# Kernel tuning notes

Measured on AMD Instinct MI355X. Metric: run time of the kernel, lower is better.

The kernel has to match this reference:

```python
import jax, jax.numpy as jnp
import numpy as np

EPS = 1e-6
H = 8  # num_heads

def _ln(x, gamma, beta):
    mu = jnp.mean(x, axis=-1, keepdims=True)
    var = jnp.mean(jnp.square(x - mu), axis=-1, keepdims=True)
    return (x - mu) * jax.lax.rsqrt(var + EPS) * gamma + beta

def setup_inputs() -> dict:
    key = jax.random.key(0)
    ks = jax.random.split(key, 10)
    b, n_sink, n_src = 2, 1024, 4096
    sink_dim, src_dim, hid = 512, 512, 512
    s = 0.02
    return {
        "sink": jax.random.normal(ks[0], (b, n_sink, sink_dim), jnp.float32),
        "source": jax.random.normal(ks[1], (b, n_src, src_dim), jnp.float32),
        "gamma_s": jnp.ones((sink_dim,), jnp.float32),
        "beta_s": jnp.zeros((sink_dim,), jnp.float32),
        "gamma_c": jnp.ones((src_dim,), jnp.float32),
        "beta_c": jnp.zeros((src_dim,), jnp.float32),
        "Wq": jax.random.normal(ks[2], (sink_dim, hid), jnp.float32) * s,
        "bq": jnp.zeros((hid,), jnp.float32),
        "Wkv": jax.random.normal(ks[3], (src_dim, 2 * hid), jnp.float32) * s,
        "bkv": jnp.zeros((2 * hid,), jnp.float32),
        "Wo": jax.random.normal(ks[4], (hid, sink_dim), jnp.float32) * s,
        "bo": jnp.zeros((sink_dim,), jnp.float32),
    }

def reference(sink, source, gamma_s, beta_s, gamma_c, beta_c, Wq, bq, Wkv, bkv, Wo, bo):
    b, n_sink, _ = sink.shape
    n_src = source.shape[1]
    hid = Wq.shape[1]
    d = hid // H
    scale = d ** -0.5
    # pre-norm
    s = _ln(sink, gamma_s, beta_s)
    c = _ln(source, gamma_c, beta_c)
    # projections -> [b, h, n, d]
    q = (s @ Wq + bq).reshape(b, n_sink, H, d).transpose(0, 2, 1, 3)
    kv = c @ Wkv + bkv
    k, v = jnp.split(kv, 2, axis=-1)
    k = k.reshape(b, n_src, H, d).transpose(0, 2, 1, 3)
    v = v.reshape(b, n_src, H, d).transpose(0, 2, 1, 3)
    sim = jnp.einsum('bhid,bhjd->bhij', q, k) * scale  # [b,h,i,j]
    # sink competition: softmax over query axis i, then renormalize over keys j
    attn = jax.nn.softmax(sim, axis=-2) + EPS
    attn = attn / jnp.sum(attn, axis=-1, keepdims=True)
    out = jnp.einsum('bhij,bhjd->bhid', attn, v)
    out = out.transpose(0, 2, 1, 3).reshape(b, n_sink, hid)
    return out @ Wo + bo
```

## Files before the change

### kernel.cpp

```cpp
#include <hip/hip_runtime.h>
#include <hip/hip_bf16.h>
#include <math.h>

#define EPS 1e-6f
#define NSINK 1024
#define NSRC 4096
#define DIM 512
#define NH 8
#define HD 64
#define BATCH 2
#define VROWS 65
#define QSCALE 0.18033688011112042f

#if __has_builtin(__builtin_amdgcn_permlane32_swap) && __has_builtin(__builtin_amdgcn_permlane16_swap)
#define HAVE_PERMLANE 1
#else
#define HAVE_PERMLANE 0
#endif

typedef unsigned short u16;
typedef __attribute__((ext_vector_type(8))) short short8;
typedef __attribute__((ext_vector_type(4))) float f32x4;

__device__ inline float fast_exp2(float x) {
#if __has_builtin(__builtin_amdgcn_exp2f)
    return __builtin_amdgcn_exp2f(x);
#else
    return exp2f(x);
#endif
}
__device__ inline float fast_rcp(float x) {
#if __has_builtin(__builtin_amdgcn_rcpf)
    return __builtin_amdgcn_rcpf(x);
#else
    return 1.0f / x;
#endif
}
__device__ inline u16 f2bf(float x) {
    union { float f; unsigned u; } v; v.f = x;
    unsigned r = v.u + 0x7fffu + ((v.u >> 16) & 1u);
    return (u16)(r >> 16);
}
__device__ inline float bf2f(u16 h) {
    union { unsigned u; float f; } v; v.u = ((unsigned)h) << 16;
    return v.f;
}
__device__ inline unsigned pk_bf16(float a, float b) {
    union { __hip_bfloat162 h; unsigned u; } v;
    v.h = __float22bfloat162_rn(make_float2(a, b));
    return v.u;
}
__device__ inline f32x4 mfma16(short8 a, short8 b, f32x4 c) {
    return __builtin_amdgcn_mfma_f32_16x16x32_bf16(a, b, c, 0, 0, 0);
}
__device__ inline short8 ldfrag(const u16* base, int stride, int lane) {
    return *(const short8*)(base + (size_t)(lane & 15) * stride + ((lane >> 4) << 3));
}

__device__ inline void gld16(const u16* g, u16* l) {
    __builtin_amdgcn_global_load_lds(
        (const __attribute__((address_space(1))) unsigned*)g,
        (__attribute__((address_space(3))) unsigned*)l, 16, 0, 0);
}

template<int TM>
__device__ inline void stage_tile(u16* lds, const u16* gsrc, int K, int t) {
    #pragma unroll
    for (int it = 0; it < TM / 32; ++it) {
        int m = it * 32 + (t >> 3);
        int c = (t & 7) ^ (m & 7);
        gld16(gsrc + (size_t)m * K + c * 8,
              lds + it * 2048 + (t >> 6) * 512);
    }
}
__device__ inline short8 rdfrag(const u16* tile, int fbase, int cbase, int lane) {
    int m = fbase + (lane & 15);
    int c = (cbase + (lane >> 4)) ^ (m & 7);
    return *(const short8*)(tile + (size_t)m * 64 + c * 8);
}

#if HAVE_PERMLANE
__device__ inline short8 pa_frag(const f32x4 sA, const f32x4 sB) {
    unsigned A0 = pk_bf16(sA[0], sA[1]);
    unsigned A1 = pk_bf16(sA[2], sA[3]);
    unsigned B0 = pk_bf16(sB[0], sB[1]);
    unsigned B1 = pk_bf16(sB[2], sB[3]);
    auto c0 = __builtin_amdgcn_permlane32_swap(A0, B0, false, false);
    auto c1 = __builtin_amdgcn_permlane32_swap(A1, B1, false, false);
    auto d0 = __builtin_amdgcn_permlane16_swap(c0[0], c0[1], false, false);
    auto d1 = __builtin_amdgcn_permlane16_swap(c1[0], c1[1], false, false);
    union { unsigned u[4]; short8 s8; } r;
    r.u[0] = d0[0]; r.u[1] = d1[0]; r.u[2] = d0[1]; r.u[3] = d1[1];
    return r.s8;
}
#endif

__global__ __launch_bounds__(256) void prep(
    const float* __restrict__ sink, const float* __restrict__ source,
    const float* __restrict__ gs, const float* __restrict__ bs,
    const float* __restrict__ gc, const float* __restrict__ bc,
    const float* __restrict__ Wq, const float* __restrict__ Wkv,
    const float* __restrict__ Wo,
    u16* __restrict__ sh, u16* __restrict__ ch,
    u16* __restrict__ wqT, u16* __restrict__ wkvT, u16* __restrict__ woT)
{
    int row = blockIdx.x;
    int t = threadIdx.x;
    if (row >= BATCH * (NSINK + NSRC)) {
        int n = row - BATCH * (NSINK + NSRC);
        const float* W; u16* T; int N; int nn;
        if (n < 512)       { W = Wq;  T = wqT;  N = 512;  nn = n; }
        else if (n < 1536) { W = Wkv; T = wkvT; N = 1024; nn = n - 512; }
        else               { W = Wo;  T = woT;  N = 512;  nn = n - 1536; }
        for (int k = t; k < 512; k += 256)
            T[(size_t)nn * 512 + k] = f2bf(W[(size_t)k * N + nn]);
        return;
    }
    const float* xr; const float* g; const float* be; u16* y;
    if (row < BATCH * NSINK) {
        xr = sink + (size_t)row * DIM; g = gs; be = bs; y = sh + (size_t)row * DIM;
    } else {
        int rr = row - BATCH * NSINK;
        xr = source + (size_t)rr * DIM; g = gc; be = bc; y = ch + (size_t)rr * DIM;
    }
    float v0 = xr[t], v1 = xr[t + 256];
    float s = v0 + v1, sq = v0 * v0 + v1 * v1;
    #pragma unroll
    for (int off = 32; off > 0; off >>= 1) {
        s  += __shfl_down(s, off, 64);
        sq += __shfl_down(sq, off, 64);
    }
    __shared__ float rsm[4], rq[4];
    int wave = t >> 6;
    if ((t & 63) == 0) { rsm[wave] = s; rq[wave] = sq; }
    __syncthreads();
    s  = rsm[0] + rsm[1] + rsm[2] + rsm[3];
    sq = rq[0] + rq[1] + rq[2] + rq[3];
    float mu = s * (1.0f / DIM);
    float var = sq * (1.0f / DIM) - mu * mu;
    float a = var + EPS;
    float r = rsqrtf(a);
    r = r * (1.5f - 0.5f * a * r * r);
    y[t]       = f2bf((v0 - mu) * r * g[t] + be[t]);
    y[t + 256] = f2bf((v1 - mu) * r * g[t + 256] + be[t + 256]);
}

template<int MODE, int TM, int TN, int SWZ>
__global__ __launch_bounds__(256) void gemm1(
    const u16* __restrict__ A, const u16* __restrict__ BT,
    const float* __restrict__ bias, int K,
    float* __restrict__ cf, u16* __restrict__ o1, u16* __restrict__ o2)
{
    constexpr int FM = TM / 32, FN = TN / 32;
    __shared__ u16 As[2][TM * 64];
    __shared__ u16 Bs[2][TN * 64];
    int t = threadIdx.x;
    int wave = t >> 6, lane = t & 63;
    int wr = wave >> 1, wc = wave & 1;
    int m0, n0;
    if constexpr (SWZ) {
        int id = blockIdx.x;
        int slot = id >> 3;
        m0 = ((id & 7) * 8 + (slot & 7)) * TM;
        n0 = (slot >> 3) * TN;
    } else {
        m0 = blockIdx.y * TM;
        n0 = blockIdx.x * TN;
    }

    f32x4 acc[FM][FN] = {};
    stage_tile<TM>(As[0], A + (size_t)m0 * K, K, t);
    stage_tile<TN>(Bs[0], BT + (size_t)n0 * K, K, t);
    __syncthreads();
    int nt = K >> 6;
    int cur = 0;
    for (int kt = 0; kt < nt; ++kt) {
        if (kt + 1 < nt) {
            stage_tile<TM>(As[cur ^ 1], A + (size_t)m0 * K + (kt + 1) * 64, K, t);
            stage_tile<TN>(Bs[cur ^ 1], BT + (size_t)n0 * K + (kt + 1) * 64, K, t);
        }
        #pragma unroll
        for (int kk = 0; kk < 2; ++kk) {
            short8 af[FM], bf[FN];
            #pragma unroll
            for (int f = 0; f < FM; ++f)
                af[f] = rdfrag(As[cur], wr * (TM / 2) + f * 16, kk * 4, lane);
            #pragma unroll
            for (int f = 0; f < FN; ++f)
                bf[f] = rdfrag(Bs[cur], wc * (TN / 2) + f * 16, kk * 4, lane);
            #pragma unroll
            for (int i = 0; i < FM; ++i)
                #pragma unroll
                for (int j = 0; j < FN; ++j)
                    acc[i][j] = mfma16(af[i], bf[j], acc[i][j]);
        }
        __syncthreads();
        cur ^= 1;
    }

    #pragma unroll
    for (int i = 0; i < FM; ++i)
        #pragma unroll
        for (int j = 0; j < FN; ++j)
            #pragma unroll
            for (int r = 0; r < 4; ++r) {
                int m = m0 + wr * (TM / 2) + i * 16 + (lane >> 4) * 4 + r;
                int n = n0 + wc * (TN / 2) + j * 16 + (lane & 15);
                float v = acc[i][j][r] + bias[n];
                if (MODE == 0) {
                    cf[(size_t)m * DIM + n] = v;
                } else if (MODE == 1) {
                    int b = m >> 10, ii = m & 1023;
                    int h = n >> 6, d = n & 63;
                    o1[((size_t)(b * NH + h) * NSINK + ii) * HD + d] = f2bf(v * QSCALE);
                } else {
                    int b = m >> 12, jj = m & 4095;
                    if (n < DIM) {
                        int h = n >> 6, d = n & 63;
                        o1[((size_t)(b * NH + h) * NSRC + jj) * HD + d] = f2bf(v);
                    } else {
                        int nn = n - DIM;
                        int h = nn >> 6, d = nn & 63;
                        o2[((size_t)(b * NH + h) * HD + d) * NSRC + jj] = f2bf(v);
                    }
                }
            }
}

__global__ __launch_bounds__(256, 4) void pass_a(const u16* __restrict__ q,
    const u16* __restrict__ k, float* __restrict__ part)
{
    int id = blockIdx.x;
    int slot = id >> 3;
    int bh = (id & 7) + 8 * (slot >> 6);
    int rem = slot & 63;
    int ic = rem >> 4;
    int t = threadIdx.x, wave = t >> 6, lane = t & 63;
    int j0 = (rem & 15) * 256 + wave * 64;
    const u16* qb = q + (size_t)bh * NSINK * HD;
    const u16* kb = k + (size_t)bh * NSRC * HD;

    __shared__ u16 Qs[2][64 * 64];

    short8 kf[4][2];
    #pragma unroll
    for (int jf = 0; jf < 4; ++jf)
        #pragma unroll
        for (int kc = 0; kc < 2; ++kc)
            kf[jf][kc] = ldfrag(kb + (size_t)(j0 + jf * 16) * HD + kc * 32, HD, lane);

    float csum[4] = {};
    stage_tile<64>(Qs[0], qb + (size_t)(ic * 256) * HD, HD, t);
    __syncthreads();
    int cur = 0;
    for (int ii = 0; ii < 4; ++ii) {
        if (ii + 1 < 4)
            stage_tile<64>(Qs[cur ^ 1], qb + (size_t)(ic * 256 + (ii + 1) * 64) * HD, HD, t);
        #pragma unroll
        for (int f = 0; f < 4; ++f) {
            short8 q0 = rdfrag(Qs[cur], f * 16, 0, lane);
            short8 q1 = rdfrag(Qs[cur], f * 16, 4, lane);
            f32x4 s[4] = {};
            #pragma unroll
            for (int jf = 0; jf < 4; ++jf) s[jf] = mfma16(q0, kf[jf][0], s[jf]);
            #pragma unroll
            for (int jf = 0; jf < 4; ++jf) s[jf] = mfma16(q1, kf[jf][1], s[jf]);
            #pragma unroll
            for (int jf = 0; jf < 4; ++jf)
                csum[jf] += fast_exp2(s[jf][0]) + fast_exp2(s[jf][1])
                          + fast_exp2(s[jf][2]) + fast_exp2(s[jf][3]);
        }
        __syncthreads();
        cur ^= 1;
    }
    #pragma unroll
    for (int jf = 0; jf < 4; ++jf) {
        csum[jf] += __shfl_xor(csum[jf], 16, 64);
        csum[jf] += __shfl_xor(csum[jf], 32, 64);
    }
    if (lane < 16)
        #pragma unroll
        for (int jf = 0; jf < 4; ++jf)
            part[((size_t)ic * BATCH * NH + bh) * NSRC + j0 + jf * 16 + lane] = csum[jf];
}

__global__ __launch_bounds__(256) void csred(const float* __restrict__ part,
    float* __restrict__ rcs)
{
    int x = blockIdx.x * 256 + threadIdx.x;
    const int S = BATCH * NH * NSRC;
    float cs = part[x] + part[x + S] + part[x + 2 * S] + part[x + 3 * S];
    rcs[x] = fast_rcp(cs);
}

__global__ __launch_bounds__(256) void vscale2(const u16* __restrict__ vTh,
    const float* __restrict__ rcs, float* __restrict__ vs, u16* __restrict__ vT2)
{
    int d = blockIdx.x;
    int bh = blockIdx.y;
    const float* rc = rcs + (size_t)bh * NSRC;
    u16* dst = vT2 + ((size_t)bh * VROWS + d) * NSRC;
    if (d == 64) {
        for (int j = threadIdx.x; j < NSRC; j += 256) dst[j] = f2bf(rc[j]);
        return;
    }
    const u16* src = vTh + ((size_t)bh * HD + d) * NSRC;
    float acc = 0.f;
    for (int j = threadIdx.x; j < NSRC; j += 256) {
        float v = bf2f(src[j]);
        acc += v;
        dst[j] = f2bf(v * rc[j]);
    }
    #pragma unroll
    for (int off = 32; off > 0; off >>= 1) acc += __shfl_down(acc, off, 64);
    __shared__ float r4[4];
    if ((threadIdx.x & 63) == 0) r4[threadIdx.x >> 6] = acc;
    __syncthreads();
    if (threadIdx.x == 0) vs[bh * HD + d] = r4[0] + r4[1] + r4[2] + r4[3];
}

__global__ __launch_bounds__(256, 3) void pass_b(const u16* __restrict__ q,
    const u16* __restrict__ k, const u16* __restrict__ vT2,
    u16* __restrict__ pvb, float* __restrict__ rs)
{
    int id = blockIdx.x;
    int slot = id >> 3;
    int bh = (id & 7) + 8 * (slot >> 5);
    int rem = slot & 31;
    int split = rem >> 3;
    int i0 = (rem & 7) * 128;
    int t = threadIdx.x, wave = t >> 6, lane = t & 63;
    const u16* qb = q + (size_t)bh * NSINK * HD;
    const u16* kb = k + (size_t)bh * NSRC * HD;
    const u16* vb = vT2 + (size_t)bh * VROWS * NSRC;

    __shared__ u16 Ks[2][64 * 64];
    __shared__ u16 Vs[2][64 * 64];
    __shared__ alignas(16) u16 Rcs[2][64];
#if !HAVE_PERMLANE
    __shared__ alignas(16) u16 pbuf[4][2][16 * 76];
#endif

    short8 qf[2][2];
    #pragma unroll
    for (int fi = 0; fi < 2; ++fi)
        #pragma unroll
        for (int kc = 0; kc < 2; ++kc)
            qf[fi][kc] = ldfrag(qb + (size_t)(i0 + wave * 32 + fi * 16) * HD + kc * 32, HD, lane);

    auto stage = [&](int buf, int jt) {
        int j0 = split * (NSRC / 4) + jt * 64;
        stage_tile<64>(Ks[buf], kb + (size_t)j0 * HD, HD, t);
        stage_tile<64>(Vs[buf], vb + j0, NSRC, t);
        if (t < 8) gld16(vb + (size_t)64 * NSRC + j0 + t * 8, Rcs[buf]);
    };

    f32x4 o[2][5] = {};
    stage(0, 0);
    __syncthreads();
    int cur = 0;
    for (int jt = 0; jt < 16; ++jt) {
        if (jt + 1 < 16) stage(cur ^ 1, jt + 1);
        f32x4 s[2][4] = {};
        #pragma unroll
        for (int kc = 0; kc < 2; ++kc)
            #pragma unroll
            for (int jf = 0; jf < 4; ++jf) {
                short8 kf = rdfrag(Ks[cur], jf * 16, kc * 4, lane);
                s[0][jf] = mfma16(kf, qf[0][kc], s[0][jf]);
                s[1][jf] = mfma16(kf, qf[1][kc], s[1][jf]);
            }
        #pragma unroll
        for (int fi = 0; fi < 2; ++fi)
            #pragma unroll
            for (int jf = 0; jf < 4; ++jf)
                #pragma unroll
                for (int r = 0; r < 4; ++r)
                    s[fi][jf][r] = fast_exp2(s[fi][jf][r]);
#if !HAVE_PERMLANE
        #pragma unroll
        for (int fi = 0; fi < 2; ++fi)
            #pragma unroll
            for (int jf = 0; jf < 4; ++jf) {
                uint2 w;
                w.x = pk_bf16(s[fi][jf][0], s[fi][jf][1]);
                w.y = pk_bf16(s[fi][jf][2], s[fi][jf][3]);
                *(uint2*)&pbuf[wave][fi][(size_t)(lane & 15) * 76 + jf * 16 + (lane >> 4) * 4] = w;
            }
#endif
        short8 z = {};
        #pragma unroll
        for (int jc = 0; jc < 2; ++jc) {
#if HAVE_PERMLANE
            short8 pa0 = pa_frag(s[0][2 * jc], s[0][2 * jc + 1]);
            short8 pa1 = pa_frag(s[1][2 * jc], s[1][2 * jc + 1]);
#else
            short8 pa0 = *(const short8*)&pbuf[wave][0][(size_t)(lane & 15) * 76 + jc * 32 + (lane >> 4) * 8];
            short8 pa1 = *(const short8*)&pbuf[wave][1][(size_t)(lane & 15) * 76 + jc * 32 + (lane >> 4) * 8];
#endif
            #pragma unroll
            for (int df = 0; df < 4; ++df) {
                short8 vf = rdfrag(Vs[cur], df * 16, jc * 4, lane);
                o[0][df] = mfma16(pa0, vf, o[0][df]);
                o[1][df] = mfma16(pa1, vf, o[1][df]);
            }
            short8 b5 = z;
            if ((lane & 15) == 0)
                b5 = *(const short8*)&Rcs[cur][jc * 32 + (lane >> 4) * 8];
            o[0][4] = mfma16(pa0, b5, o[0][4]);
            o[1][4] = mfma16(pa1, b5, o[1][4]);
        }
        __syncthreads();
        cur ^= 1;
    }
    if ((lane & 15) == 0) {
        #pragma unroll
        for (int fi = 0; fi < 2; ++fi)
            #pragma unroll
            for (int r = 0; r < 4; ++r)
                rs[((size_t)split * (BATCH * NH) + bh) * NSINK + i0 + wave * 32 + fi * 16 + (lane >> 4) * 4 + r] = o[fi][4][r];
    }
    int b = bh >> 3, h = bh & 7;
    u16* pvp = pvb + (size_t)split * BATCH * NSINK * DIM;
    #pragma unroll
    for (int fi = 0; fi < 2; ++fi)
        #pragma unroll
        for (int df = 0; df < 4; ++df)
            #pragma unroll
            for (int r = 0; r < 4; ++r) {
                int row = i0 + wave * 32 + fi * 16 + (lane >> 4) * 4 + r;
                pvp[((size_t)(b * NSINK + row)) * DIM + h * HD + df * 16 + (lane & 15)] = f2bf(o[fi][df][r]);
            }
}

__global__ __launch_bounds__(256) void finalize_pv(const u16* __restrict__ pvb,
    const float* __restrict__ rs, const float* __restrict__ vs,
    u16* __restrict__ ab)
{
    const int M = BATCH * NSINK * DIM;
    const int R = BATCH * NH * NSINK;
    int idx = blockIdx.x * 256 + threadIdx.x;
    int m = idx >> 9, n = idx & 511;
    int b = m >> 10, i = m & 1023, h = n >> 6, d = n & 63;
    int bh = b * NH + h;
    float val = bf2f(pvb[idx]) + bf2f(pvb[idx + M]) + bf2f(pvb[idx + 2 * M])
              + bf2f(pvb[idx + 3 * M]) + EPS * vs[bh * HD + d];
    float rsv = rs[bh * NSINK + i] + rs[R + bh * NSINK + i]
              + rs[2 * R + bh * NSINK + i] + rs[3 * R + bh * NSINK + i]
              + (float)NSRC * EPS;
    ab[idx] = f2bf(val / rsv);
}

extern "C" void kernel_launch(void* const* d_in, const int* in_sizes, int n_in,
                              void* d_out, int out_size, void* d_ws, size_t ws_size,
                              hipStream_t stream) {
    (void)in_sizes; (void)n_in; (void)out_size;
    const float* sink    = (const float*)d_in[0];
    const float* source  = (const float*)d_in[1];
    const float* gamma_s = (const float*)d_in[2];
    const float* beta_s  = (const float*)d_in[3];
    const float* gamma_c = (const float*)d_in[4];
    const float* beta_c  = (const float*)d_in[5];
    const float* Wq      = (const float*)d_in[6];
    const float* bq      = (const float*)d_in[7];
    const float* Wkv     = (const float*)d_in[8];
    const float* bkv     = (const float*)d_in[9];
    const float* Wo      = (const float*)d_in[10];
    const float* bo      = (const float*)d_in[11];
    float* out = (float*)d_out;

    char* p = (char*)d_ws;
    auto carve = [&](size_t bytes) { char* r = p; p += (bytes + 255) & ~(size_t)255; return r; };
    u16* sh    = (u16*)carve(2048ull * 512 * 2);
    u16* ch    = (u16*)carve(8192ull * 512 * 2);
    u16* wqT   = (u16*)carve(512ull * 512 * 2);
    u16* wkvT  = (u16*)carve(1024ull * 512 * 2);
    u16* woT   = (u16*)carve(512ull * 512 * 2);
    u16* qb    = (u16*)carve(16ull * 1024 * 64 * 2);
    u16* kb    = (u16*)carve(16ull * 4096 * 64 * 2);
    u16* vTh   = (u16*)carve(16ull * 64 * 4096 * 2);
    u16* vT2   = (u16*)carve(16ull * VROWS * 4096 * 2);
    float* cs_part = (float*)carve(4ull * 16 * 4096 * 4);
    float* rcs     = (float*)carve(16ull * 4096 * 4);
    float* vs      = (float*)carve(1024ull * 4);
    float* rs      = (float*)carve(4ull * 16 * 1024 * 4);
    u16*   pvb     = (u16*)carve(4ull * 2048 * 512 * 2);
    u16*   ab      = (u16*)carve(2048ull * 512 * 2);
    if ((size_t)(p - (char*)d_ws) > ws_size) return;

    prep<<<BATCH * (NSINK + NSRC) + 2048, 256, 0, stream>>>(
        sink, source, gamma_s, beta_s, gamma_c, beta_c,
        Wq, Wkv, Wo, sh, ch, wqT, wkvT, woT);

    gemm1<1, 64, 64, 0><<<dim3(DIM / 64, BATCH * NSINK / 64), 256, 0, stream>>>(
        sh, wqT, bq, 512, nullptr, qb, nullptr);
    gemm1<2, 128, 128, 1><<<512, 256, 0, stream>>>(
        ch, wkvT, bkv, 512, nullptr, kb, vTh);

    pass_a<<<1024, 256, 0, stream>>>(qb, kb, cs_part);
    csred<<<BATCH * NH * NSRC / 256, 256, 0, stream>>>(cs_part, rcs);
    vscale2<<<dim3(VROWS, BATCH * NH), 256, 0, stream>>>(vTh, rcs, vs, vT2);
    pass_b<<<512, 256, 0, stream>>>(qb, kb, vT2, pvb, rs);
    finalize_pv<<<4096, 256, 0, stream>>>(pvb, rs, vs, ab);

    gemm1<0, 64, 64, 0><<<dim3(DIM / 64, BATCH * NSINK / 64), 256, 0, stream>>>(
        ab, woT, bo, 512, out, nullptr, nullptr);
}
```

Before: 106.4 us.

## Apply column reciprocal inside pass_b instead of pre-scaling V

Removes the vscale2 kernel that wrote a pre-scaled V copy plus a reciprocal row, and folds the column-sum reciprocal into pass_b by multiplying the exponentiated scores by an fp32 reciprocal tile staged in shared memory. The row-sum accumulation now multiplies by a constant ones fragment. csred and the V column-sum are merged into one launch. This saves one launch and a full read/write pass over V, at the cost of extra multiplies in the pass_b inner loop and slightly different rounding, since the scale is applied before the bf16 pack.

```diff
diff --git a/kernel.cpp b/kernel.cpp
--- a/kernel.cpp
+++ b/kernel.cpp
@@ -9,7 +9,6 @@
 #define NH 8
 #define HD 64
 #define BATCH 2
-#define VROWS 65
 #define QSCALE 0.18033688011112042f
 
 #if __has_builtin(__builtin_amdgcn_permlane32_swap) && __has_builtin(__builtin_amdgcn_permlane16_swap)
@@ -284,44 +283,32 @@
             part[((size_t)ic * BATCH * NH + bh) * NSRC + j0 + jf * 16 + lane] = csum[jf];
 }
 
-__global__ __launch_bounds__(256) void csred(const float* __restrict__ part,
-    float* __restrict__ rcs)
-{
-    int x = blockIdx.x * 256 + threadIdx.x;
-    const int S = BATCH * NH * NSRC;
-    float cs = part[x] + part[x + S] + part[x + 2 * S] + part[x + 3 * S];
-    rcs[x] = fast_rcp(cs);
-}
-
-__global__ __launch_bounds__(256) void vscale2(const u16* __restrict__ vTh,
-    const float* __restrict__ rcs, float* __restrict__ vs, u16* __restrict__ vT2)
-{
-    int d = blockIdx.x;
-    int bh = blockIdx.y;
-    const float* rc = rcs + (size_t)bh * NSRC;
-    u16* dst = vT2 + ((size_t)bh * VROWS + d) * NSRC;
-    if (d == 64) {
-        for (int j = threadIdx.x; j < NSRC; j += 256) dst[j] = f2bf(rc[j]);
+__global__ __launch_bounds__(256) void csred_vsum(const float* __restrict__ part,
+    const u16* __restrict__ vTh, float* __restrict__ rcs, float* __restrict__ vs)
+{
+    int blk = blockIdx.x;
+    if (blk < 256) {
+        int x = blk * 256 + threadIdx.x;
+        const int S = BATCH * NH * NSRC;
+        float cs = part[x] + part[x + S] + part[x + 2 * S] + part[x + 3 * S];
+        rcs[x] = fast_rcp(cs);
         return;
     }
-    const u16* src = vTh + ((size_t)bh * HD + d) * NSRC;
-    float acc = 0.f;
-    for (int j = threadIdx.x; j < NSRC; j += 256) {
-        float v = bf2f(src[j]);
-        acc += v;
-        dst[j] = f2bf(v * rc[j]);
-    }
-    #pragma unroll
-    for (int off = 32; off > 0; off >>= 1) acc += __shfl_down(acc, off, 64);
+    int row = blk - 256;
+    const u16* ph = vTh + (size_t)row * NSRC;
+    float s = 0.f;
+    for (int j = threadIdx.x; j < NSRC; j += 256) s += bf2f(ph[j]);
+    #pragma unroll
+    for (int off = 32; off > 0; off >>= 1) s += __shfl_down(s, off, 64);
     __shared__ float r4[4];
-    if ((threadIdx.x & 63) == 0) r4[threadIdx.x >> 6] = acc;
+    if ((threadIdx.x & 63) == 0) r4[threadIdx.x >> 6] = s;
     __syncthreads();
-    if (threadIdx.x == 0) vs[bh * HD + d] = r4[0] + r4[1] + r4[2] + r4[3];
+    if (threadIdx.x == 0) vs[row] = r4[0] + r4[1] + r4[2] + r4[3];
 }
 
 __global__ __launch_bounds__(256, 3) void pass_b(const u16* __restrict__ q,
-    const u16* __restrict__ k, const u16* __restrict__ vT2,
-    u16* __restrict__ pvb, float* __restrict__ rs)
+    const u16* __restrict__ k, const u16* __restrict__ vTh,
+    const float* __restrict__ rcs, u16* __restrict__ pvb, float* __restrict__ rs)
 {
     int id = blockIdx.x;
     int slot = id >> 3;
@@ -332,11 +319,12 @@
     int t = threadIdx.x, wave = t >> 6, lane = t & 63;
     const u16* qb = q + (size_t)bh * NSINK * HD;
     const u16* kb = k + (size_t)bh * NSRC * HD;
-    const u16* vb = vT2 + (size_t)bh * VROWS * NSRC;
+    const u16* vb = vTh + (size_t)bh * HD * NSRC;
+    const float* rc = rcs + (size_t)bh * NSRC;
 
     __shared__ u16 Ks[2][64 * 64];
     __shared__ u16 Vs[2][64 * 64];
-    __shared__ alignas(16) u16 Rcs[2][64];
+    __shared__ alignas(16) float RcsF[2][64];
 #if !HAVE_PERMLANE
     __shared__ alignas(16) u16 pbuf[4][2][16 * 76];
 #endif
@@ -347,12 +335,18 @@
         #pragma unroll
         for (int kc = 0; kc < 2; ++kc)
             qf[fi][kc] = ldfrag(qb + (size_t)(i0 + wave * 32 + fi * 16) * HD + kc * 32, HD, lane);
+
+    short8 ones8;
+    #pragma unroll
+    for (int i = 0; i < 8; ++i) ones8[i] = (short)0x3F80;
+    short8 z = {};
+    short8 b5 = ((lane & 15) == 0) ? ones8 : z;
 
     auto stage = [&](int buf, int jt) {
         int j0 = split * (NSRC / 4) + jt * 64;
         stage_tile<64>(Ks[buf], kb + (size_t)j0 * HD, HD, t);
         stage_tile<64>(Vs[buf], vb + j0, NSRC, t);
-        if (t < 8) gld16(vb + (size_t)64 * NSRC + j0 + t * 8, Rcs[buf]);
+        if (t < 16) gld16((const u16*)(rc + j0) + t * 8, (u16*)RcsF[buf]);
     };
 
     f32x4 o[2][5] = {};
@@ -371,12 +365,14 @@
                 s[1][jf] = mfma16(kf, qf[1][kc], s[1][jf]);
             }
         #pragma unroll
-        for (int fi = 0; fi < 2; ++fi)
-            #pragma unroll
-            for (int jf = 0; jf < 4; ++jf)
+        for (int jf = 0; jf < 4; ++jf) {
+            f32x4 rcv = *(const f32x4*)&RcsF[cur][jf * 16 + ((lane >> 4) << 2)];
+            #pragma unroll
+            for (int fi = 0; fi < 2; ++fi)
                 #pragma unroll
                 for (int r = 0; r < 4; ++r)
-                    s[fi][jf][r] = fast_exp2(s[fi][jf][r]);
+                    s[fi][jf][r] = fast_exp2(s[fi][jf][r]) * rcv[r];
+        }
 #if !HAVE_PERMLANE
         #pragma unroll
         for (int fi = 0; fi < 2; ++fi)
@@ -388,7 +384,6 @@
                 *(uint2*)&pbuf[wave][fi][(size_t)(lane & 15) * 76 + jf * 16 + (lane >> 4) * 4] = w;
             }
 #endif
-        short8 z = {};
         #pragma unroll
         for (int jc = 0; jc < 2; ++jc) {
 #if HAVE_PERMLANE
@@ -404,9 +399,6 @@
                 o[0][df] = mfma16(pa0, vf, o[0][df]);
                 o[1][df] = mfma16(pa1, vf, o[1][df]);
             }
-            short8 b5 = z;
-            if ((lane & 15) == 0)
-                b5 = *(const short8*)&Rcs[cur][jc * 32 + (lane >> 4) * 8];
             o[0][4] = mfma16(pa0, b5, o[0][4]);
             o[1][4] = mfma16(pa1, b5, o[1][4]);
         }
@@ -479,7 +471,6 @@
     u16* qb    = (u16*)carve(16ull * 1024 * 64 * 2);
     u16* kb    = (u16*)carve(16ull * 4096 * 64 * 2);
     u16* vTh   = (u16*)carve(16ull * 64 * 4096 * 2);
-    u16* vT2   = (u16*)carve(16ull * VROWS * 4096 * 2);
     float* cs_part = (float*)carve(4ull * 16 * 4096 * 4);
     float* rcs     = (float*)carve(16ull * 4096 * 4);
     float* vs      = (float*)carve(1024ull * 4);
@@ -498,9 +489,8 @@
         ch, wkvT, bkv, 512, nullptr, kb, vTh);
 
     pass_a<<<1024, 256, 0, stream>>>(qb, kb, cs_part);
-    csred<<<BATCH * NH * NSRC / 256, 256, 0, stream>>>(cs_part, rcs);
-    vscale2<<<dim3(VROWS, BATCH * NH), 256, 0, stream>>>(vTh, rcs, vs, vT2);
-    pass_b<<<512, 256, 0, stream>>>(qb, kb, vT2, pvb, rs);
+    csred_vsum<<<256 + 1024, 256, 0, stream>>>(cs_part, vTh, rcs, vs);
+    pass_b<<<512, 256, 0, stream>>>(qb, kb, vTh, rcs, pvb, rs);
     finalize_pv<<<4096, 256, 0, stream>>>(pvb, rs, vs, ab);
 
     gemm1<0, 64, 64, 0><<<dim3(DIM / 64, BATCH * NSINK / 64), 256, 0, stream>>>(
```

After: 106.6 us. No clear change (+0.2%).
